# Performance work log

Hardware: AMD Instinct MI355X
Metric: run time of the kernel (lower is better)

Reference implementation:

```python
import jax, jax.numpy as jnp
import numpy as np

B, DIN, DP, DOUT, K, N = 4, 64, 3, 64, 16, 8192


def setup_inputs() -> dict:
    key = jax.random.key(0)
    ks = jax.random.split(key, 5)
    features = jax.random.normal(ks[0], (B, DIN, N), dtype=jnp.float32)
    positions = jax.random.normal(ks[1], (B, DP, N), dtype=jnp.float32)
    neighborhoods = jax.random.randint(ks[2], (B, K, N), 0, N, dtype=jnp.int32)
    position_theta = jax.random.normal(ks[3], (DP, DIN, DOUT), dtype=jnp.float32) * 0.05
    position_bias = jnp.zeros((DIN, DOUT), dtype=jnp.float32)
    feature_bias = jnp.zeros((DOUT, 1), dtype=jnp.float32)
    return {
        "features": features,
        "positions": positions,
        "neighborhoods": neighborhoods,
        "position_theta": position_theta,
        "position_bias": position_bias,
        "feature_bias": feature_bias,
    }


def _gather_neighbors(x, idx):
    # x: [D, N], idx: [K, N] -> [D, K, N]
    return x[:, idx]


def reference(features, positions, neighborhoods, position_theta, position_bias, feature_bias):
    # Gather neighbor features/positions: [B, D, K, N]
    fg = jax.vmap(_gather_neighbors)(features, neighborhoods)      # [B, Din, K, N]
    pg = jax.vmap(_gather_neighbors)(positions, neighborhoods)     # [B, Dp,  K, N]
    # Relative positions of neighbors w.r.t. center point
    rel = pg - positions[:, :, None, :]                            # [B, Dp, K, N]
    # Dynamic weight w[b,k,n] = theta . rel + bias, contracted with
    # gathered features and summed over K, without materializing [Din,Dout] per neighbor.
    y = jnp.einsum('pio,bpkn,bikn->bon', position_theta, rel, fg)
    y = y + jnp.einsum('io,bikn->bon', position_bias, fg)
    # feature bias [Dout, 1] broadcasts over [B, Dout, N]
    y = y + feature_bias[None, :, :]
    return y  # [B, Dout, N]; activation=None (linear)
```

## Files before the change

### kernel.cpp

```cpp
#include <hip/hip_runtime.h>

#define NB    4
#define DIN_  64
#define DOUT_ 64
#define KN    16
#define NPT   8192
#define CPAD  264

typedef __attribute__((ext_vector_type(8))) short short8;
typedef __attribute__((ext_vector_type(4))) float v4f;

__device__ __forceinline__ float bf2f(unsigned short u) {
    unsigned int x = ((unsigned int)u) << 16;
    float f; __builtin_memcpy(&f, &x, 4); return f;
}
__device__ __forceinline__ unsigned short f2bf(float f) {
    unsigned int x; __builtin_memcpy(&x, &f, 4);
    x += 0x7fffu + ((x >> 16) & 1u);
    return (unsigned short)(x >> 16);
}

__global__ void k_prep(const float* __restrict__ feat, const float* __restrict__ pos,
                       const float* __restrict__ theta, const float* __restrict__ pbias,
                       unsigned short* __restrict__ ft, float4* __restrict__ pt,
                       unsigned short* __restrict__ tbf) {
    __shared__ float tile[64][65];
    const int bid = blockIdx.x;
    if (bid < 512) {
        int b = bid >> 7, n0 = (bid & 127) << 6;
        int lane = threadIdx.x & 63, w = threadIdx.x >> 6;
#pragma unroll
        for (int r = 0; r < 16; ++r) {
            int i = (r << 2) | w;
            tile[i][lane] = feat[(b*DIN_ + i)*NPT + n0 + lane];
        }
        __syncthreads();
#pragma unroll
        for (int r = 0; r < 16; ++r) {
            int n = (r << 2) | w;
            ft[((size_t)(b*NPT + n0 + n))*DIN_ + lane] = f2bf(tile[lane][n]);
        }
    } else if (bid < 640) {
        int t = (bid - 512)*256 + threadIdx.x;
        int b = t >> 13, n = t & 8191;
        float4 v;
        v.x = pos[(b*3 + 0)*NPT + n];
        v.y = pos[(b*3 + 1)*NPT + n];
        v.z = pos[(b*3 + 2)*NPT + n];
        v.w = 1.0f;
        pt[t] = v;
    } else {
        int e = (bid - 640)*256 + threadIdx.x;
        int o = e >> 5, g = e & 31;
        short8 u;
#pragma unroll
        for (int j = 0; j < 8; ++j) {
            int c = g*8 + j;
            float v = (c < 192) ? theta[c*64 + o] : pbias[(c - 192)*64 + o];
            u[j] = (short)f2bf(v);
        }
        *reinterpret_cast<short8*>(tbf + o*256 + g*8) = u;
    }
}

template<bool USE_WS>
__global__ __launch_bounds__(256, 4) void k_main(
    const float*          __restrict__ feat,
    const float*          __restrict__ pos,
    const int*            __restrict__ nbr,
    const float*          __restrict__ theta,
    const float*          __restrict__ pbias,
    const float*          __restrict__ fbias,
    const unsigned short* __restrict__ ft,
    const float4*         __restrict__ pt,
    const unsigned short* __restrict__ tbf,
    float*                __restrict__ out)
{
    __shared__ __align__(16) unsigned short Xt[32*CPAD];

    const int tid  = threadIdx.x;
    const int lane = tid & 63;
    const int w    = tid >> 6;
    const int j8   = lane & 7;
    const int pq   = lane >> 3;

    const int base = blockIdx.x << 5;
    const int b    = base >> 13;
    const int nb0  = base & 8191;
    const int q    = (w << 3) + pq;
    const int n    = nb0 + q;

    const unsigned short* ftb = ft + (((size_t)b) << 19);
    const float4*         ptb = pt + b*NPT;

    float4 pc;
    if (USE_WS) pc = ptb[n];
    else {
        pc.x = pos[(b*3+0)*NPT + n];
        pc.y = pos[(b*3+1)*NPT + n];
        pc.z = pos[(b*3+2)*NPT + n];
        pc.w = 1.0f;
    }

    float acc[4][8];
#pragma unroll
    for (int p = 0; p < 4; ++p)
#pragma unroll
        for (int j = 0; j < 8; ++j) acc[p][j] = 0.f;

#pragma unroll
    for (int k = 0; k < KN; ++k) {
        const int id = nbr[(b*KN + k)*NPT + n];
        float4 pg; float f[8];
        if (USE_WS) {
            pg = ptb[id];
            short8 fr = *reinterpret_cast<const short8*>(
                ftb + (((size_t)id) << 6) + (j8 << 3));
#pragma unroll
            for (int j = 0; j < 8; ++j) f[j] = bf2f((unsigned short)fr[j]);
        } else {
            pg.x = pos[(b*3+0)*NPT + id];
            pg.y = pos[(b*3+1)*NPT + id];
            pg.z = pos[(b*3+2)*NPT + id];
            pg.w = 1.0f;
#pragma unroll
            for (int j = 0; j < 8; ++j)
                f[j] = feat[(b*DIN_ + (j8<<3) + j)*NPT + id];
        }
#pragma unroll
        for (int j = 0; j < 8; ++j) {
            acc[0][j] += pg.x * f[j];
            acc[1][j] += pg.y * f[j];
            acc[2][j] += pg.z * f[j];
            acc[3][j] += f[j];
        }
    }
#pragma unroll
    for (int j = 0; j < 8; ++j) {
        acc[0][j] -= pc.x * acc[3][j];
        acc[1][j] -= pc.y * acc[3][j];
        acc[2][j] -= pc.z * acc[3][j];
    }
#pragma unroll
    for (int p = 0; p < 4; ++p) {
        short8 pk;
#pragma unroll
        for (int j = 0; j < 8; ++j) pk[j] = (short)f2bf(acc[p][j]);
        *reinterpret_cast<short8*>(&Xt[q*CPAD + (p<<6) + (j8<<3)]) = pk;
    }
    __syncthreads();

    const int j16 = lane & 15;
    const int kg  = lane >> 4;
    const int orow = (w << 4) + j16;
    v4f acc0 = {0.f,0.f,0.f,0.f}, acc1 = {0.f,0.f,0.f,0.f};
#pragma unroll
    for (int ks = 0; ks < 8; ++ks) {
        const int koff = (ks << 5) + (kg << 3);
        short8 a;
        if (USE_WS) {
            a = *reinterpret_cast<const short8*>(tbf + orow*256 + koff);
        } else {
#pragma unroll
            for (int j = 0; j < 8; ++j) {
                int c = koff + j;
                float v = (c < 192) ? theta[c*64 + orow] : pbias[(c - 192)*64 + orow];
                a[j] = (short)f2bf(v);
            }
        }
        short8 b0 = *reinterpret_cast<const short8*>(&Xt[j16*CPAD + koff]);
        short8 b1 = *reinterpret_cast<const short8*>(&Xt[(16 + j16)*CPAD + koff]);
        acc0 = __builtin_amdgcn_mfma_f32_16x16x32_bf16(a, b0, acc0, 0, 0, 0);
        acc1 = __builtin_amdgcn_mfma_f32_16x16x32_bf16(a, b1, acc1, 0, 0, 0);
    }
#pragma unroll
    for (int r = 0; r < 4; ++r) {
        const int o = (w << 4) + (kg << 2) + r;
        const float fb = fbias[o];
        const size_t rowoff = (size_t)(b*DOUT_ + o)*NPT + nb0;
        out[rowoff + j16]      = acc0[r] + fb;
        out[rowoff + 16 + j16] = acc1[r] + fb;
    }
}

extern "C" void kernel_launch(void* const* d_in, const int* in_sizes, int n_in,
                              void* d_out, int out_size, void* d_ws, size_t ws_size,
                              hipStream_t stream) {
    const float* feat  = (const float*)d_in[0];
    const float* pos   = (const float*)d_in[1];
    const int*   nbr   = (const int*)d_in[2];
    const float* theta = (const float*)d_in[3];
    const float* pbias = (const float*)d_in[4];
    const float* fbias = (const float*)d_in[5];
    float* out = (float*)d_out;

    const size_t ft_bytes  = (size_t)NB*NPT*DIN_*2;
    const size_t pt_bytes  = (size_t)NB*NPT*sizeof(float4);
    const size_t tbf_bytes = (size_t)DOUT_*256*2;
    const int n_blocks = (NB*NPT)/32;

    if (ws_size >= ft_bytes + pt_bytes + tbf_bytes) {
        unsigned short* ft  = (unsigned short*)d_ws;
        float4*         pt  = (float4*)((char*)d_ws + ft_bytes);
        unsigned short* tbf = (unsigned short*)((char*)d_ws + ft_bytes + pt_bytes);
        k_prep<<<648, 256, 0, stream>>>(feat, pos, theta, pbias, ft, pt, tbf);
        k_main<true><<<n_blocks, 256, 0, stream>>>(feat, pos, nbr, theta, pbias, fbias,
                                                   ft, pt, tbf, out);
    } else {
        k_main<false><<<n_blocks, 256, 0, stream>>>(feat, pos, nbr, theta, pbias, fbias,
                                                    (const unsigned short*)feat,
                                                    (const float4*)feat,
                                                    (const unsigned short*)feat, out);
    }
}
```

Measured before the change: 91.73 us.

## Fuse prep and main kernels via cooperative launch with grid sync

```diff
diff --git a/kernel.cpp b/kernel.cpp
--- a/kernel.cpp
+++ b/kernel.cpp
@@ -1,4 +1,7 @@
 #include <hip/hip_runtime.h>
+#include <hip/hip_cooperative_groups.h>
+
+namespace cg = cooperative_groups;
 
 #define NB    4
 #define DIN_  64
@@ -6,6 +9,7 @@
 #define KN    16
 #define NPT   8192
 #define CPAD  264
+#define SMEM_BYTES 16896
 
 typedef __attribute__((ext_vector_type(8))) short short8;
 typedef __attribute__((ext_vector_type(4))) float v4f;
@@ -20,15 +24,16 @@
     return (unsigned short)(x >> 16);
 }
 
-__global__ void k_prep(const float* __restrict__ feat, const float* __restrict__ pos,
-                       const float* __restrict__ theta, const float* __restrict__ pbias,
-                       unsigned short* __restrict__ ft, float4* __restrict__ pt,
-                       unsigned short* __restrict__ tbf) {
-    __shared__ float tile[64][65];
-    const int bid = blockIdx.x;
+__device__ __forceinline__ void prep_work(int bid, int tid,
+    const float* __restrict__ feat, const float* __restrict__ pos,
+    const float* __restrict__ theta, const float* __restrict__ pbias,
+    unsigned short* __restrict__ ft, float4* __restrict__ pt,
+    unsigned short* __restrict__ tbf, void* smem)
+{
     if (bid < 512) {
+        float (*tile)[65] = reinterpret_cast<float(*)[65]>(smem);
         int b = bid >> 7, n0 = (bid & 127) << 6;
-        int lane = threadIdx.x & 63, w = threadIdx.x >> 6;
+        int lane = tid & 63, w = tid >> 6;
 #pragma unroll
         for (int r = 0; r < 16; ++r) {
             int i = (r << 2) | w;
@@ -41,7 +46,7 @@
             ft[((size_t)(b*NPT + n0 + n))*DIN_ + lane] = f2bf(tile[lane][n]);
         }
     } else if (bid < 640) {
-        int t = (bid - 512)*256 + threadIdx.x;
+        int t = (bid - 512)*256 + tid;
         int b = t >> 13, n = t & 8191;
         float4 v;
         v.x = pos[(b*3 + 0)*NPT + n];
@@ -49,8 +54,8 @@
         v.z = pos[(b*3 + 2)*NPT + n];
         v.w = 1.0f;
         pt[t] = v;
-    } else {
-        int e = (bid - 640)*256 + threadIdx.x;
+    } else if (bid < 648) {
+        int e = (bid - 640)*256 + tid;
         int o = e >> 5, g = e & 31;
         short8 u;
 #pragma unroll
@@ -64,27 +69,21 @@
 }
 
 template<bool USE_WS>
-__global__ __launch_bounds__(256, 4) void k_main(
-    const float*          __restrict__ feat,
-    const float*          __restrict__ pos,
-    const int*            __restrict__ nbr,
-    const float*          __restrict__ theta,
-    const float*          __restrict__ pbias,
-    const float*          __restrict__ fbias,
-    const unsigned short* __restrict__ ft,
-    const float4*         __restrict__ pt,
-    const unsigned short* __restrict__ tbf,
-    float*                __restrict__ out)
+__device__ __forceinline__ void main_work(int bid, int tid,
+    const float* __restrict__ feat, const float* __restrict__ pos,
+    const int* __restrict__ nbr, const float* __restrict__ theta,
+    const float* __restrict__ pbias, const float* __restrict__ fbias,
+    const unsigned short* __restrict__ ft, const float4* __restrict__ pt,
+    const unsigned short* __restrict__ tbf, float* __restrict__ out, void* smem)
 {
-    __shared__ __align__(16) unsigned short Xt[32*CPAD];
-
-    const int tid  = threadIdx.x;
+    unsigned short* Xt = (unsigned short*)smem;
+
     const int lane = tid & 63;
     const int w    = tid >> 6;
     const int j8   = lane & 7;
     const int pq   = lane >> 3;
 
-    const int base = blockIdx.x << 5;
+    const int base = bid << 5;
     const int b    = base >> 13;
     const int nb0  = base & 8191;
     const int q    = (w << 3) + pq;
@@ -102,15 +101,20 @@
         pc.w = 1.0f;
     }
 
+    int ids[KN];
+#pragma unroll
+    for (int k = 0; k < KN; ++k)
+        ids[k] = nbr[(b*KN + k)*NPT + n];
+
     float acc[4][8];
 #pragma unroll
     for (int p = 0; p < 4; ++p)
 #pragma unroll
         for (int j = 0; j < 8; ++j) acc[p][j] = 0.f;
 
-#pragma unroll
+#pragma unroll 4
     for (int k = 0; k < KN; ++k) {
-        const int id = nbr[(b*KN + k)*NPT + n];
+        const int id = ids[k];
         float4 pg; float f[8];
         if (USE_WS) {
             pg = ptb[id];
@@ -181,6 +185,40 @@
         out[rowoff + j16]      = acc0[r] + fb;
         out[rowoff + 16 + j16] = acc1[r] + fb;
     }
+}
+
+__global__ void k_prep(const float* __restrict__ feat, const float* __restrict__ pos,
+                       const float* __restrict__ theta, const float* __restrict__ pbias,
+                       unsigned short* __restrict__ ft, float4* __restrict__ pt,
+                       unsigned short* __restrict__ tbf) {
+    __shared__ __align__(16) unsigned char smem[SMEM_BYTES];
+    prep_work(blockIdx.x, threadIdx.x, feat, pos, theta, pbias, ft, pt, tbf, smem);
+}
+
+template<bool USE_WS>
+__global__ __launch_bounds__(256, 4) void k_main(
+    const float* __restrict__ feat, const float* __restrict__ pos,
+    const int* __restrict__ nbr, const float* __restrict__ theta,
+    const float* __restrict__ pbias, const float* __restrict__ fbias,
+    const unsigned short* __restrict__ ft, const float4* __restrict__ pt,
+    const unsigned short* __restrict__ tbf, float* __restrict__ out) {
+    __shared__ __align__(16) unsigned char smem[SMEM_BYTES];
+    main_work<USE_WS>(blockIdx.x, threadIdx.x, feat, pos, nbr, theta, pbias, fbias,
+                      ft, pt, tbf, out, smem);
+}
+
+__global__ __launch_bounds__(256, 4) void k_fused(
+    const float* __restrict__ feat, const float* __restrict__ pos,
+    const int* __restrict__ nbr, const float* __restrict__ theta,
+    const float* __restrict__ pbias, const float* __restrict__ fbias,
+    unsigned short* __restrict__ ft, float4* __restrict__ pt,
+    unsigned short* __restrict__ tbf, float* __restrict__ out) {
+    __shared__ __align__(16) unsigned char smem[SMEM_BYTES];
+    prep_work(blockIdx.x, threadIdx.x, feat, pos, theta, pbias, ft, pt, tbf, smem);
+    __threadfence();
+    cg::this_grid().sync();
+    main_work<true>(blockIdx.x, threadIdx.x, feat, pos, nbr, theta, pbias, fbias,
+                    ft, pt, tbf, out, smem);
 }
 
 extern "C" void kernel_launch(void* const* d_in, const int* in_sizes, int n_in,
@@ -203,6 +241,18 @@
         unsigned short* ft  = (unsigned short*)d_ws;
         float4*         pt  = (float4*)((char*)d_ws + ft_bytes);
         unsigned short* tbf = (unsigned short*)((char*)d_ws + ft_bytes + pt_bytes);
+
+        int coop = 0;
+        (void)hipDeviceGetAttribute(&coop, hipDeviceAttributeCooperativeLaunch, 0);
+        if (coop) {
+            void* args[] = {(void*)&feat, (void*)&pos, (void*)&nbr, (void*)&theta,
+                            (void*)&pbias, (void*)&fbias, (void*)&ft, (void*)&pt,
+                            (void*)&tbf, (void*)&out};
+            hipError_t e = hipLaunchCooperativeKernel((const void*)k_fused,
+                                                      dim3(n_blocks), dim3(256),
+                                                      args, 0, stream);
+            if (e == hipSuccess) return;
+        }
         k_prep<<<648, 256, 0, stream>>>(feat, pos, theta, pbias, ft, pt, tbf);
         k_main<true><<<n_blocks, 256, 0, stream>>>(feat, pos, nbr, theta, pbias, fbias,
                                                    ft, pt, tbf, out);
```

After: 298.2 us. +225.1%, slower.
